# Kernel optimization log

Hardware: AMD Instinct MI355X
Metric: run time of the kernel (lower is better)

## Reference

```python
import jax, jax.numpy as jnp
import numpy as np

N = 50000        # nodes
E = 800000       # edges (before self-loops)
IN = 512         # in_channels
HEADS = 8        # 'head' arg: heads and per-head out dim of conv1
C1 = 8           # per-head channels of conv1 (== head)
OUT = 128        # out_channels of conv2
NEG_SLOPE = 0.2  # PyG GATConv leaky-relu slope


def _glorot(key, shape, fan_in):
    return jax.random.normal(key, shape, jnp.float32) * (1.0 / np.sqrt(fan_in))


def setup_inputs() -> dict:
    key = jax.random.key(0)
    ks = jax.random.split(key, 10)
    x = jax.random.normal(ks[0], (N, IN), jnp.float32)
    edge_index = jax.random.randint(ks[1], (2, E), 0, N, dtype=jnp.int32)
    # conv1: GATConv(IN, C1, heads=HEADS, concat=True)
    W1 = _glorot(ks[2], (IN, HEADS * C1), IN)
    att_src1 = _glorot(ks[3], (HEADS, C1), C1)
    att_dst1 = _glorot(ks[4], (HEADS, C1), C1)
    bias1 = jnp.zeros((HEADS * C1,), jnp.float32)
    # conv2: GATConv(HEADS*C1, OUT, heads=1, concat=False)
    W2 = _glorot(ks[5], (HEADS * C1, OUT), HEADS * C1)
    att_src2 = _glorot(ks[6], (1, OUT), OUT)
    att_dst2 = _glorot(ks[7], (1, OUT), OUT)
    bias2 = jnp.zeros((OUT,), jnp.float32)
    return {"x": x, "edge_index": edge_index,
            "W1": W1, "att_src1": att_src1, "att_dst1": att_dst1, "bias1": bias1,
            "W2": W2, "att_src2": att_src2, "att_dst2": att_dst2, "bias2": bias2}


def gat_conv(x, src, dst, W, a_src, a_dst, bias, heads, concat):
    """PyG GATConv (eval mode, dropout off). src/dst already include self-loops."""
    n = x.shape[0]
    h = (x @ W).reshape(n, heads, -1)                 # [N, H, C]
    s = (h * a_src[None]).sum(-1)                     # [N, H] alpha_src per node
    d = (h * a_dst[None]).sum(-1)                     # [N, H] alpha_dst per node
    alpha = jax.nn.leaky_relu(s[src] + d[dst], NEG_SLOPE)  # [E, H]
    # segment softmax over incoming edges of each destination node
    amax = jax.ops.segment_max(alpha, dst, num_segments=n)  # [N, H]
    amax = jnp.where(jnp.isfinite(amax), amax, 0.0)
    ea = jnp.exp(alpha - amax[dst])                   # [E, H]
    denom = jax.ops.segment_sum(ea, dst, num_segments=n)
    w = ea / (denom[dst] + 1e-16)                     # [E, H]
    msg = h[src] * w[..., None]                       # [E, H, C]
    out = jax.ops.segment_sum(msg, dst, num_segments=n)  # [N, H, C]
    out = out.reshape(n, -1) if concat else out.mean(axis=1)
    return out + bias


def reference(x, edge_index, W1, att_src1, att_dst1, bias1,
              W2, att_src2, att_dst2, bias2):
    n = x.shape[0]
    loop = jnp.arange(n, dtype=edge_index.dtype)      # PyG adds self-loops
    src = jnp.concatenate([edge_index[0], loop])
    dst = jnp.concatenate([edge_index[1], loop])
    h = jax.nn.elu(gat_conv(x, src, dst, W1, att_src1, att_dst1, bias1,
                            heads=HEADS, concat=True))
    out = jax.nn.elu(gat_conv(h, src, dst, W2, att_src2, att_dst2, bias2,
                              heads=1, concat=False))
    return out
```

## Files before the change

### kernel.cpp

```cpp
#include <hip/hip_runtime.h>

#define NEG_SLOPE 0.2f
#define CAP 128

typedef __attribute__((ext_vector_type(8))) short bf16x8;
typedef __attribute__((ext_vector_type(4))) float f32x4;

__device__ __forceinline__ float leaky(float v) {
    return v > 0.0f ? v : NEG_SLOPE * v;
}
__device__ __forceinline__ float elu(float v) {
    return v > 0.0f ? v : (__expf(v) - 1.0f);
}
__device__ __forceinline__ short f2b(float f) {
    return (short)((__float_as_uint(f) + 0x8000u) >> 16);
}
__device__ __forceinline__ float bf2f(unsigned short v) {
    return __uint_as_float(((unsigned)v) << 16);
}

__global__ void prep_k(const float* __restrict__ W1, const float* __restrict__ W2,
                       unsigned short* __restrict__ w1s, unsigned short* __restrict__ w2s,
                       int* __restrict__ wp, int N) {
    int i = blockIdx.x * 256 + threadIdx.x;
    if (i < N) wp[i] = 0;
    if (i < 512 * 64) {
        int k = i >> 6, n = i & 63;
        int kt = k >> 5, kk = k & 31;
        int nt = n >> 4, nn = n & 15;
        int lane = (kk >> 3) * 16 + nn, j = kk & 7;
        w1s[(((size_t)(kt * 4 + nt)) * 64 + lane) * 8 + j] = (unsigned short)f2b(W1[i]);
    } else if (i < 512 * 64 + 64 * 128) {
        int i2 = i - 512 * 64;
        int k = i2 >> 7, n = i2 & 127;
        int kt = k >> 5, kk = k & 31;
        int nt = n >> 4, nn = n & 15;
        int lane = (kk >> 3) * 16 + nn, j = kk & 7;
        w2s[(((size_t)(kt * 8 + nt)) * 64 + lane) * 8 + j] = (unsigned short)f2b(W2[i2]);
    }
}

__global__ __launch_bounds__(256) void gemm1_k(const float* __restrict__ X,
                                               const unsigned short* __restrict__ Ws,
                                               const float* __restrict__ Asrc,
                                               const float* __restrict__ Adst,
                                               unsigned short* __restrict__ Hb,
                                               float* __restrict__ S,
                                               float* __restrict__ D, int N) {
    const int lane = threadIdx.x & 63;
    const int wave = threadIdx.x >> 6;
    const int m0 = blockIdx.x * 64 + wave * 16;
    const int q = lane >> 4, lc = lane & 15;
    const int arow = m0 + lc;
    const float* xrow = X + (size_t)min(arow, N - 1) * 512 + q * 8;
    const bf16x8* bW = (const bf16x8*)Ws;

    f32x4 acc[4] = {{0.f,0.f,0.f,0.f},{0.f,0.f,0.f,0.f},{0.f,0.f,0.f,0.f},{0.f,0.f,0.f,0.f}};

    for (int g = 0; g < 4; ++g) {
        float4 a[8];
#pragma unroll
        for (int u = 0; u < 8; ++u)
            a[u] = *(const float4*)(xrow + g * 128 + (u >> 1) * 32 + (u & 1) * 4);
#pragma unroll
        for (int u2 = 0; u2 < 4; ++u2) {
            const int kt = g * 4 + u2;
            float4 a0 = a[u2 * 2], a1 = a[u2 * 2 + 1];
            bf16x8 af;
            af[0] = f2b(a0.x); af[1] = f2b(a0.y); af[2] = f2b(a0.z); af[3] = f2b(a0.w);
            af[4] = f2b(a1.x); af[5] = f2b(a1.y); af[6] = f2b(a1.z); af[7] = f2b(a1.w);
#pragma unroll
            for (int nt = 0; nt < 4; ++nt) {
                bf16x8 bf = bW[(size_t)(kt * 4 + nt) * 64 + lane];
                acc[nt] = __builtin_amdgcn_mfma_f32_16x16x32_bf16(af, bf, acc[nt], 0, 0, 0);
            }
        }
    }

    float asc[4], adc[4];
#pragma unroll
    for (int nt = 0; nt < 4; ++nt) { asc[nt] = Asrc[nt * 16 + lc]; adc[nt] = Adst[nt * 16 + lc]; }

#pragma unroll
    for (int r = 0; r < 4; ++r) {
        int row = m0 + q * 4 + r;
        bool ok = row < N;
        if (ok) {
#pragma unroll
            for (int nt = 0; nt < 4; ++nt)
                Hb[(size_t)row * 64 + nt * 16 + lc] = (unsigned short)f2b(acc[nt][r]);
        }
        float ps[4], pd[4];
#pragma unroll
        for (int nt = 0; nt < 4; ++nt) { ps[nt] = acc[nt][r] * asc[nt]; pd[nt] = acc[nt][r] * adc[nt]; }
#pragma unroll
        for (int off = 1; off < 8; off <<= 1) {
#pragma unroll
            for (int nt = 0; nt < 4; ++nt) {
                ps[nt] += __shfl_xor(ps[nt], off);
                pd[nt] += __shfl_xor(pd[nt], off);
            }
        }
        if (ok && !(lc & 7)) {
            int hb = lc >> 3;
#pragma unroll
            for (int nt = 0; nt < 4; ++nt) {
                S[(size_t)row * 8 + nt * 2 + hb] = ps[nt];
                D[(size_t)row * 8 + nt * 2 + hb] = pd[nt];
            }
        }
    }
}

__global__ void pack_k(const int* __restrict__ ei, int E,
                       int* __restrict__ wp, int* __restrict__ srcs) {
    int base = (blockIdx.x * blockDim.x + threadIdx.x) * 4;
    if (base + 4 <= E) {
        int4 s = *(const int4*)(ei + base);
        int4 d = *(const int4*)(ei + E + base);
        int c0 = atomicAdd(&wp[d.x], 1);
        int c1 = atomicAdd(&wp[d.y], 1);
        int c2 = atomicAdd(&wp[d.z], 1);
        int c3 = atomicAdd(&wp[d.w], 1);
        if (c0 < CAP) srcs[((size_t)d.x << 7) + c0] = s.x;
        if (c1 < CAP) srcs[((size_t)d.y << 7) + c1] = s.y;
        if (c2 < CAP) srcs[((size_t)d.z << 7) + c2] = s.z;
        if (c3 < CAP) srcs[((size_t)d.w << 7) + c3] = s.w;
    } else {
        for (int e = base; e < E; ++e) {
            int dd = ei[E + e];
            int c = atomicAdd(&wp[dd], 1);
            if (c < CAP) srcs[((size_t)dd << 7) + c] = ei[e];
        }
    }
}

__global__ __launch_bounds__(256) void agg1g2_k(const int* __restrict__ wp,
                                                const int* __restrict__ srcs,
                                                const float* __restrict__ S1,
                                                const float* __restrict__ D1,
                                                const unsigned short* __restrict__ H1b,
                                                const float* __restrict__ b1,
                                                const unsigned short* __restrict__ W2s,
                                                const float* __restrict__ as2,
                                                const float* __restrict__ ad2,
                                                unsigned short* __restrict__ H2b,
                                                float* __restrict__ S2,
                                                float* __restrict__ D2, int N) {
    __shared__ unsigned short sh[16][64];
    __shared__ float shp[4][16], shq[4][16];

    const int tid  = threadIdx.x;
    const int lane = tid & 63;
    const int wave = tid >> 6;
    const int m0 = blockIdx.x * 16;

    const int h = lane & 7;
    const int el = lane >> 3;
#pragma unroll
    for (int rep = 0; rep < 4; ++rep) {
        const int nl = wave * 4 + rep;
        const int wid = m0 + nl;
        if (wid < N) {
            const int deg = min(wp[wid], CAP);
            const size_t b0 = (size_t)wid << 7;
            const float dvh = D1[(size_t)wid * 8 + h];

            float wself = __expf(leaky(S1[(size_t)wid * 8 + h] + dvh));
            float den = (el == 0) ? wself : 0.0f;
            float acc = __shfl(wself, lane >> 3) * bf2f(H1b[(size_t)wid * 64 + lane]);

            for (int base = 0; base < deg; base += 8) {
                int i = base + el;
                int src_l = 0; float w_l = 0.0f;
                if (i < deg) {
                    src_l = srcs[b0 + i];
                    w_l = __expf(leaky(S1[(size_t)src_l * 8 + h] + dvh));
                }
                den += w_l;
#pragma unroll
                for (int j = 0; j < 8; ++j) {
                    float w = __shfl(w_l, j * 8 + (lane >> 3));
                    int src = __builtin_amdgcn_readfirstlane(__shfl(src_l, j * 8));
                    acc += w * bf2f(H1b[(size_t)src * 64 + lane]);
                }
            }
#pragma unroll
            for (int off = 8; off < 64; off <<= 1)
                den += __shfl_xor(den, off);
            float rden = 1.0f / (__shfl(den, lane >> 3) + 1e-16f);
            sh[nl][lane] = (unsigned short)f2b(elu(acc * rden + b1[lane]));
        } else {
            sh[nl][lane] = 0;
        }
    }
    __syncthreads();

    const int q = lane >> 4, lc = lane & 15;
    const bf16x8* bW = (const bf16x8*)W2s;
    const int nt0 = wave * 2;

    f32x4 acc2[2] = {{0.f,0.f,0.f,0.f},{0.f,0.f,0.f,0.f}};
#pragma unroll
    for (int kt = 0; kt < 2; ++kt) {
        bf16x8 af = *(const bf16x8*)(&sh[lc][q * 8 + kt * 32]);
#pragma unroll
        for (int u = 0; u < 2; ++u) {
            bf16x8 bf = bW[(size_t)(kt * 8 + nt0 + u) * 64 + lane];
            acc2[u] = __builtin_amdgcn_mfma_f32_16x16x32_bf16(af, bf, acc2[u], 0, 0, 0);
        }
    }
    float asc[2], adc[2];
#pragma unroll
    for (int u = 0; u < 2; ++u) {
        asc[u] = as2[(nt0 + u) * 16 + lc];
        adc[u] = ad2[(nt0 + u) * 16 + lc];
    }
#pragma unroll
    for (int r = 0; r < 4; ++r) {
        int rl = q * 4 + r;
        int row = m0 + rl;
        if (row < N) {
#pragma unroll
            for (int u = 0; u < 2; ++u)
                H2b[(size_t)row * 128 + (nt0 + u) * 16 + lc] = (unsigned short)f2b(acc2[u][r]);
        }
        float ps = acc2[0][r] * asc[0] + acc2[1][r] * asc[1];
        float pd = acc2[0][r] * adc[0] + acc2[1][r] * adc[1];
#pragma unroll
        for (int off = 1; off < 16; off <<= 1) {
            ps += __shfl_xor(ps, off);
            pd += __shfl_xor(pd, off);
        }
        if (lc == 0) { shp[wave][rl] = ps; shq[wave][rl] = pd; }
    }
    __syncthreads();
    if (tid < 16) {
        int row = m0 + tid;
        if (row < N) {
            float s = shp[0][tid] + shp[1][tid] + shp[2][tid] + shp[3][tid];
            float d = shq[0][tid] + shq[1][tid] + shq[2][tid] + shq[3][tid];
            S2[row] = s;
            D2[row] = d;
        }
    }
}

__global__ __launch_bounds__(256) void agg2_k(const int* __restrict__ wp,
                                              const int* __restrict__ srcs,
                                              const float* __restrict__ S,
                                              const float* __restrict__ D,
                                              const unsigned short* __restrict__ Hb,
                                              const float* __restrict__ bias,
                                              float* __restrict__ out, int N) {
    const int wid = (blockIdx.x * 256 + threadIdx.x) >> 6;
    const int lane = threadIdx.x & 63;
    if (wid >= N) return;
    const int deg = min(wp[wid], CAP);
    const size_t b0 = (size_t)wid << 7;
    const float dv = D[wid];
    const int c0 = lane * 2;

    const float wself = __expf(leaky(S[wid] + dv));
    float den = (lane == 0) ? wself : 0.0f;
    float acc0, acc1;
    {
        unsigned pv = *(const unsigned*)(Hb + (size_t)wid * 128 + c0);
        acc0 = wself * __uint_as_float(pv << 16);
        acc1 = wself * __uint_as_float(pv & 0xffff0000u);
    }

    for (int base = 0; base < deg; base += 64) {
        int i = base + lane;
        int src_l = 0; float w_l = 0.0f;
        if (i < deg) {
            src_l = srcs[b0 + i];
            w_l = __expf(leaky(S[src_l] + dv));
        }
        den += w_l;
        const int cnt = min(64, deg - base);
        for (int j0 = 0; j0 < cnt; j0 += 8) {
#pragma unroll
            for (int u = 0; u < 8; ++u) {
                int j = j0 + u;
                float w = __shfl(w_l, j);
                int src = __builtin_amdgcn_readfirstlane(__shfl(src_l, j));
                unsigned pv = *(const unsigned*)(Hb + (size_t)src * 128 + c0);
                acc0 += w * __uint_as_float(pv << 16);
                acc1 += w * __uint_as_float(pv & 0xffff0000u);
            }
        }
    }
#pragma unroll
    for (int off = 1; off < 64; off <<= 1)
        den += __shfl_xor(den, off);
    const float rden = 1.0f / (den + 1e-16f);
    float2 o;
    o.x = elu(acc0 * rden + bias[c0]);
    o.y = elu(acc1 * rden + bias[c0 + 1]);
    *(float2*)(out + (size_t)wid * 128 + c0) = o;
}

extern "C" void kernel_launch(void* const* d_in, const int* in_sizes, int n_in,
                              void* d_out, int out_size, void* d_ws, size_t ws_size,
                              hipStream_t stream) {
    const float* x   = (const float*)d_in[0];
    const int*   ei  = (const int*)d_in[1];
    const float* W1  = (const float*)d_in[2];
    const float* as1 = (const float*)d_in[3];
    const float* ad1 = (const float*)d_in[4];
    const float* b1  = (const float*)d_in[5];
    const float* W2  = (const float*)d_in[6];
    const float* as2 = (const float*)d_in[7];
    const float* ad2 = (const float*)d_in[8];
    const float* b2  = (const float*)d_in[9];

    const int N = in_sizes[0] / 512;
    const int E = in_sizes[1] / 2;

    unsigned short* w1s  = (unsigned short*)d_ws;
    unsigned short* w2s  = w1s + 512 * 64;
    unsigned short* h1b  = w2s + 64 * 128;
    unsigned short* h2b  = h1b + (size_t)N * 64;
    float*          s1   = (float*)(h2b + (size_t)N * 128);
    float*          d1   = s1 + (size_t)N * 8;
    float*          s2   = d1 + (size_t)N * 8;
    float*          d2   = s2 + N;
    int*            wp   = (int*)(d2 + N);
    int*            srcs = wp + N;

    const int B = 256;
    const int gblk = (N + 63) / 64;
    int prep_n = 512 * 64 + 64 * 128;
    if (N > prep_n) prep_n = N;

    prep_k<<<(prep_n + B - 1) / B, B, 0, stream>>>(W1, W2, w1s, w2s, wp, N);
    gemm1_k<<<gblk, B, 0, stream>>>(x, w1s, as1, ad1, h1b, s1, d1, N);
    pack_k<<<(E + B * 4 - 1) / (B * 4), B, 0, stream>>>(ei, E, wp, srcs);
    agg1g2_k<<<(N + 15) / 16, B, 0, stream>>>(wp, srcs, s1, d1, h1b, b1,
                                              w2s, as2, ad2, h2b, s2, d2, N);
    agg2_k<<<(N + 3) / 4, B, 0, stream>>>(wp, srcs, s2, d2, h2b, b2,
                                          (float*)d_out, N);
}
```

Measured before the change: 334.1 us.

## Restructure layer-1 aggregation to per-edge-group vector gathers, simplify pack, deepen GEMM prefetch

The layer-1 aggregation now gives each 8-lane group its own edge and has each lane gather a 16-byte bf16x8 slice of that source's features. The old loop broadcast one source per step and read it with 64 scalar loads. Partial sums are combined with a cross-group shuffle reduction, which adds shuffle work and register pressure. The pack kernel now handles one edge per thread instead of four to spread the atomics over more threads. The GEMM loop loads 16 float4 values per stage instead of 8, putting more loads in flight at the cost of more registers.

```diff
diff --git a/kernel.cpp b/kernel.cpp
--- a/kernel.cpp
+++ b/kernel.cpp
@@ -57,14 +57,14 @@
 
     f32x4 acc[4] = {{0.f,0.f,0.f,0.f},{0.f,0.f,0.f,0.f},{0.f,0.f,0.f,0.f},{0.f,0.f,0.f,0.f}};
 
-    for (int g = 0; g < 4; ++g) {
-        float4 a[8];
-#pragma unroll
-        for (int u = 0; u < 8; ++u)
-            a[u] = *(const float4*)(xrow + g * 128 + (u >> 1) * 32 + (u & 1) * 4);
-#pragma unroll
-        for (int u2 = 0; u2 < 4; ++u2) {
-            const int kt = g * 4 + u2;
+    for (int g = 0; g < 2; ++g) {
+        float4 a[16];
+#pragma unroll
+        for (int u = 0; u < 16; ++u)
+            a[u] = *(const float4*)(xrow + g * 256 + (u >> 1) * 32 + (u & 1) * 4);
+#pragma unroll
+        for (int u2 = 0; u2 < 8; ++u2) {
+            const int kt = g * 8 + u2;
             float4 a0 = a[u2 * 2], a1 = a[u2 * 2 + 1];
             bf16x8 af;
             af[0] = f2b(a0.x); af[1] = f2b(a0.y); af[2] = f2b(a0.z); af[3] = f2b(a0.w);
@@ -112,26 +112,14 @@
     }
 }
 
-__global__ void pack_k(const int* __restrict__ ei, int E,
-                       int* __restrict__ wp, int* __restrict__ srcs) {
-    int base = (blockIdx.x * blockDim.x + threadIdx.x) * 4;
-    if (base + 4 <= E) {
-        int4 s = *(const int4*)(ei + base);
-        int4 d = *(const int4*)(ei + E + base);
-        int c0 = atomicAdd(&wp[d.x], 1);
-        int c1 = atomicAdd(&wp[d.y], 1);
-        int c2 = atomicAdd(&wp[d.z], 1);
-        int c3 = atomicAdd(&wp[d.w], 1);
-        if (c0 < CAP) srcs[((size_t)d.x << 7) + c0] = s.x;
-        if (c1 < CAP) srcs[((size_t)d.y << 7) + c1] = s.y;
-        if (c2 < CAP) srcs[((size_t)d.z << 7) + c2] = s.z;
-        if (c3 < CAP) srcs[((size_t)d.w << 7) + c3] = s.w;
-    } else {
-        for (int e = base; e < E; ++e) {
-            int dd = ei[E + e];
-            int c = atomicAdd(&wp[dd], 1);
-            if (c < CAP) srcs[((size_t)dd << 7) + c] = ei[e];
-        }
+__global__ __launch_bounds__(256) void pack_k(const int* __restrict__ ei, int E,
+                                              int* __restrict__ wp, int* __restrict__ srcs) {
+    int e = blockIdx.x * 256 + threadIdx.x;
+    if (e < E) {
+        int s = ei[e];
+        int d = ei[E + e];
+        int c = atomicAdd(&wp[d], 1);
+        if (c < CAP) srcs[((size_t)d << 7) + c] = s;
     }
 }
 
@@ -156,7 +144,7 @@
     const int m0 = blockIdx.x * 16;
 
     const int h = lane & 7;
-    const int el = lane >> 3;
+    const int eg = lane >> 3;
 #pragma unroll
     for (int rep = 0; rep < 4; ++rep) {
         const int nl = wave * 4 + rep;
@@ -167,31 +155,43 @@
             const float dvh = D1[(size_t)wid * 8 + h];
 
             float wself = __expf(leaky(S1[(size_t)wid * 8 + h] + dvh));
-            float den = (el == 0) ? wself : 0.0f;
-            float acc = __shfl(wself, lane >> 3) * bf2f(H1b[(size_t)wid * 64 + lane]);
+            float den = (eg == 0) ? wself : 0.0f;
+            float acc[8] = {0.f,0.f,0.f,0.f,0.f,0.f,0.f,0.f};
+            if (eg == 0) {
+                bf16x8 hv = *(const bf16x8*)(H1b + (size_t)wid * 64 + h * 8);
+#pragma unroll
+                for (int c = 0; c < 8; ++c)
+                    acc[c] = wself * bf2f((unsigned short)hv[c]);
+            }
 
             for (int base = 0; base < deg; base += 8) {
-                int i = base + el;
-                int src_l = 0; float w_l = 0.0f;
-                if (i < deg) {
-                    src_l = srcs[b0 + i];
-                    w_l = __expf(leaky(S1[(size_t)src_l * 8 + h] + dvh));
-                }
-                den += w_l;
-#pragma unroll
-                for (int j = 0; j < 8; ++j) {
-                    float w = __shfl(w_l, j * 8 + (lane >> 3));
-                    int src = __builtin_amdgcn_readfirstlane(__shfl(src_l, j * 8));
-                    acc += w * bf2f(H1b[(size_t)src * 64 + lane]);
-                }
-            }
-#pragma unroll
-            for (int off = 8; off < 64; off <<= 1)
+                int i = base + eg;
+                bool v = i < deg;
+                int src = v ? srcs[b0 + i] : wid;
+                float w = v ? __expf(leaky(S1[(size_t)src * 8 + h] + dvh)) : 0.0f;
+                den += w;
+                bf16x8 hv = *(const bf16x8*)(H1b + (size_t)src * 64 + h * 8);
+#pragma unroll
+                for (int c = 0; c < 8; ++c)
+                    acc[c] += w * bf2f((unsigned short)hv[c]);
+            }
+#pragma unroll
+            for (int off = 8; off < 64; off <<= 1) {
                 den += __shfl_xor(den, off);
-            float rden = 1.0f / (__shfl(den, lane >> 3) + 1e-16f);
-            sh[nl][lane] = (unsigned short)f2b(elu(acc * rden + b1[lane]));
-        } else {
-            sh[nl][lane] = 0;
+#pragma unroll
+                for (int c = 0; c < 8; ++c)
+                    acc[c] += __shfl_xor(acc[c], off);
+            }
+            if (eg == 0) {
+                const float rden = 1.0f / (den + 1e-16f);
+                bf16x8 o;
+#pragma unroll
+                for (int c = 0; c < 8; ++c)
+                    o[c] = f2b(elu(acc[c] * rden + b1[h * 8 + c]));
+                *(bf16x8*)(&sh[nl][h * 8]) = o;
+            }
+        } else if (eg == 0) {
+            *(bf16x8*)(&sh[nl][h * 8]) = bf16x8{0,0,0,0,0,0,0,0};
         }
     }
     __syncthreads();
@@ -336,7 +336,7 @@
 
     prep_k<<<(prep_n + B - 1) / B, B, 0, stream>>>(W1, W2, w1s, w2s, wp, N);
     gemm1_k<<<gblk, B, 0, stream>>>(x, w1s, as1, ad1, h1b, s1, d1, N);
-    pack_k<<<(E + B * 4 - 1) / (B * 4), B, 0, stream>>>(ei, E, wp, srcs);
+    pack_k<<<(E + B - 1) / B, B, 0, stream>>>(ei, E, wp, srcs);
     agg1g2_k<<<(N + 15) / 16, B, 0, stream>>>(wp, srcs, s1, d1, h1b, b1,
                                               w2s, as2, ad2, h2b, s2, d2, N);
     agg2_k<<<(N + 3) / 4, B, 0, stream>>>(wp, srcs, s2, d2, h2b, b2,
```

After: 317.9 us. -4.8%, faster.
